# Performance work log

Hardware: AMD Instinct MI355X
Metric: run time of the kernel (lower is better)

Reference implementation:

```python
import jax, jax.numpy as jnp
import numpy as np

B, N, E, H = 32, 512, 512, 8
DH = E // H  # head dim = 64


def setup_inputs() -> dict:
    key = jax.random.key(0)
    ks = jax.random.split(key, 10)
    x = jax.random.normal(ks[0], (B, N, E), jnp.float32)
    adj = jax.random.bernoulli(ks[1], 0.5, (N, N))
    # ensure every query attends to at least itself (no fully-masked rows)
    adj = adj.at[jnp.arange(N), jnp.arange(N)].set(True)
    s = 0.02
    Wq = s * jax.random.normal(ks[2], (E, E), jnp.float32)
    Wk = s * jax.random.normal(ks[3], (E, E), jnp.float32)
    Wv = s * jax.random.normal(ks[4], (E, E), jnp.float32)
    Wo = s * jax.random.normal(ks[5], (E, E), jnp.float32)
    bq = s * jax.random.normal(ks[6], (E,), jnp.float32)
    bk = s * jax.random.normal(ks[7], (E,), jnp.float32)
    bv = s * jax.random.normal(ks[8], (E,), jnp.float32)
    bo = s * jax.random.normal(ks[9], (E,), jnp.float32)
    return {"x": x, "adj": adj, "Wq": Wq, "Wk": Wk, "Wv": Wv,
            "bq": bq, "bk": bk, "bv": bv, "Wo": Wo, "bo": bo}


def reference(x, adj, Wq, Wk, Wv, bq, bk, bv, Wo, bo):
    # Original module loops over queries i, calling nn.MultiheadAttention with
    # key_padding_mask = ~adj[i]; equivalent to one attention with ~adj as a
    # per-query x per-key mask (True = disallowed).
    b, n, e = x.shape
    mask = ~adj  # [N,N] True where attention is NOT allowed
    q = (x @ Wq.T + bq).reshape(b, n, H, DH)
    k = (x @ Wk.T + bk).reshape(b, n, H, DH)
    v = (x @ Wv.T + bv).reshape(b, n, H, DH)
    scale = 1.0 / jnp.sqrt(jnp.float32(DH))
    scores = jnp.einsum('bqhd,bkhd->bhqk', q, k) * scale  # [B,H,N,N]
    scores = jnp.where(mask[None, None, :, :], -jnp.inf, scores)
    p = jax.nn.softmax(scores, axis=-1)
    o = jnp.einsum('bhqk,bkhd->bqhd', p, v).reshape(b, n, e)
    return o @ Wo.T + bo  # [B,N,E]
```

## Files before the change

kernel.cpp:

```cpp
#include <hip/hip_runtime.h>
#include <stdint.h>

typedef __bf16 bf16_t;
typedef bf16_t bf16x8 __attribute__((ext_vector_type(8)));
typedef float f32x4 __attribute__((ext_vector_type(4)));


__device__ __forceinline__ uint16_t f2bf(float f) {
    uint32_t u = __float_as_uint(f);
    u += 0x7FFFu + ((u >> 16) & 1u);
    return (uint16_t)(u >> 16);
}

__device__ __forceinline__ f32x4 mfma16(bf16x8 a, bf16x8 b, f32x4 c) {
    return __builtin_amdgcn_mfma_f32_16x16x32_bf16(a, b, c, 0, 0, 0);
}

__device__ __forceinline__ bf16x8 lds_frag(const uint16_t* smem, int row, int kbyte) {
    int off = row * 128 + (kbyte ^ ((row & 7) << 4));
    return __builtin_bit_cast(bf16x8,
        *reinterpret_cast<const uint4*>(reinterpret_cast<const char*>(smem) + off));
}

template <int ROWS>
__device__ __forceinline__ void stage_tile(uint16_t* lds, const uint16_t* src,
                                           int src_stride, int tid) {
    constexpr int CH  = ROWS * 8;
    constexpr int PER = CH / 256;
#pragma unroll
    for (int i = 0; i < PER; ++i) {
        int c   = tid + i * 256;
        int row = c >> 3, cc = c & 7;
        uint4 v = *reinterpret_cast<const uint4*>(src + (size_t)row * src_stride + cc * 8);
        int off = row * 128 + ((cc * 16) ^ ((row & 7) << 4));
        *reinterpret_cast<uint4*>(reinterpret_cast<char*>(lds) + off) = v;
    }
}

__global__ void detect_kernel(const unsigned int* __restrict__ adj, int* __restrict__ flag) {
    __shared__ int notint, notf32;
    if (threadIdx.x == 0) { notint = 0; notf32 = 0; }
    __syncthreads();
    int ni = 0, nf = 0;
    for (int i = threadIdx.x; i < 4096; i += 256) {
        unsigned v = adj[i];
        if (v > 1u) ni = 1;
        if (v != 0u && v != 0x3f800000u) nf = 1;
    }
    if (ni) notint = 1;
    if (nf) notf32 = 1;
    __syncthreads();
    if (threadIdx.x == 0) *flag = notint ? (notf32 ? 2 : 1) : 0;
}

__global__ void convert_kernel(const float* __restrict__ x, const float* __restrict__ wq,
                               const float* __restrict__ wk, const float* __restrict__ wv,
                               const float* __restrict__ wo,
                               uint16_t* __restrict__ xb, uint16_t* __restrict__ wqb,
                               uint16_t* __restrict__ wkb, uint16_t* __restrict__ wvb,
                               uint16_t* __restrict__ wob) {
    int i = blockIdx.x * 256 + threadIdx.x;
    const float* src; uint16_t* dst; int idx;
    if (i < 2097152) { src = x; dst = xb; idx = i; }
    else {
        int wi = i - 2097152;
        int which = wi >> 16; idx = wi & 65535;
        src = which == 0 ? wq : which == 1 ? wk : which == 2 ? wv : wo;
        dst = which == 0 ? wqb : which == 1 ? wkb : which == 2 ? wvb : wob;
    }
    float4 v = reinterpret_cast<const float4*>(src)[idx];
    ushort4 o;
    o.x = f2bf(v.x); o.y = f2bf(v.y); o.z = f2bf(v.z); o.w = f2bf(v.w);
    reinterpret_cast<ushort4*>(dst)[idx] = o;
}

template <int MODE>
__launch_bounds__(256)
__global__ void gemm_kernel(const uint16_t* __restrict__ A,
                            const uint16_t* __restrict__ B0, const uint16_t* __restrict__ B1,
                            const uint16_t* __restrict__ B2,
                            const float* __restrict__ bias0, const float* __restrict__ bias1,
                            const float* __restrict__ bias2,
                            uint16_t* __restrict__ qws, uint16_t* __restrict__ kws,
                            uint16_t* __restrict__ vws, float* __restrict__ outf) {
    __shared__ uint16_t As[128 * 64];
    __shared__ uint16_t Bs[128 * 64];
    const int tid  = threadIdx.x;
    const int lane = tid & 63;
    const int wid  = tid >> 6;
    const int wm   = wid >> 1, wn = wid & 1;
    const int m0   = blockIdx.y * 128;
    const int n0   = blockIdx.x * 128;
    const int sel  = n0 >> 9;
    const int nw   = n0 & 511;
    const uint16_t* Bsrc = (MODE == 0) ? (sel == 0 ? B0 : sel == 1 ? B1 : B2) : B0;
    const int fr = lane & 15, fq = lane >> 4;

    f32x4 acc[4][4];
#pragma unroll
    for (int a = 0; a < 4; ++a)
#pragma unroll
        for (int b = 0; b < 4; ++b) acc[a][b] = (f32x4){0.f, 0.f, 0.f, 0.f};

    for (int k0 = 0; k0 < 512; k0 += 64) {
        __syncthreads();
        stage_tile<128>(As, A + (size_t)m0 * 512 + k0, 512, tid);
        stage_tile<128>(Bs, Bsrc + (size_t)nw * 512 + k0, 512, tid);
        __syncthreads();
#pragma unroll
        for (int ks = 0; ks < 2; ++ks) {
            int kb = ks * 64 + fq * 16;
            bf16x8 af[4], bfr[4];
#pragma unroll
            for (int i = 0; i < 4; ++i) af[i]  = lds_frag(As, wm * 64 + i * 16 + fr, kb);
#pragma unroll
            for (int i = 0; i < 4; ++i) bfr[i] = lds_frag(Bs, wn * 64 + i * 16 + fr, kb);
#pragma unroll
            for (int mf = 0; mf < 4; ++mf)
#pragma unroll
                for (int nf = 0; nf < 4; ++nf)
                    acc[mf][nf] = mfma16(af[mf], bfr[nf], acc[mf][nf]);
        }
    }

    if (MODE == 0) {
        const float* bias = sel == 0 ? bias0 : sel == 1 ? bias1 : bias2;
#pragma unroll
        for (int nf = 0; nf < 4; ++nf) {
            int c  = nw + wn * 64 + nf * 16 + fr;
            float bv = bias[c];
            int h = c >> 6, dh = c & 63;
#pragma unroll
            for (int mf = 0; mf < 4; ++mf) {
                int mbase = m0 + wm * 64 + mf * 16 + fq * 4;
                int b  = mbase >> 9;
                int ns = mbase & 511;
                if (sel < 2) {
                    uint16_t* dst = (sel == 0 ? qws : kws);
                    size_t base = ((size_t)(b * 8 + h) * 512) * 64;
#pragma unroll
                    for (int j = 0; j < 4; ++j)
                        dst[base + (size_t)(ns + j) * 64 + dh] = f2bf(acc[mf][nf][j] + bv);
                } else {
                    ushort4 pk;
                    pk.x = f2bf(acc[mf][nf][0] + bv);
                    pk.y = f2bf(acc[mf][nf][1] + bv);
                    pk.z = f2bf(acc[mf][nf][2] + bv);
                    pk.w = f2bf(acc[mf][nf][3] + bv);
                    *reinterpret_cast<ushort4*>(
                        &vws[((size_t)(b * 8 + h) * 64 + dh) * 512 + ns]) = pk;
                }
            }
        }
    } else {
#pragma unroll
        for (int nf = 0; nf < 4; ++nf) {
            int c = n0 + wn * 64 + nf * 16 + fr;
            float bv = bias0[c];
#pragma unroll
            for (int mf = 0; mf < 4; ++mf) {
                int mbase = m0 + wm * 64 + mf * 16 + fq * 4;
#pragma unroll
                for (int j = 0; j < 4; ++j)
                    outf[(size_t)(mbase + j) * 512 + c] = acc[mf][nf][j] + bv;
            }
        }
    }
}

__launch_bounds__(256)
__global__ void attn_kernel(const uint16_t* __restrict__ qws, const uint16_t* __restrict__ kws,
                            const uint16_t* __restrict__ vws, const void* __restrict__ adj,
                            const int* __restrict__ mode_flag, uint16_t* __restrict__ ows) {
    __shared__ uint16_t Ks[64 * 64];
    __shared__ uint16_t Vs[64 * 64];
    __shared__ uint16_t Ps[4 * 16 * 64];
    const int tid = threadIdx.x, lane = tid & 63, w = tid >> 6;
    const int bx = blockIdx.x;
    const int qt = bx & 7, h = (bx >> 3) & 7, b = bx >> 6;
    const int mode = *mode_flag;
    const size_t qk_head = (size_t)(b * 8 + h) * 512 * 64;
    const size_t v_head  = (size_t)(b * 8 + h) * 64 * 512;
    const int fr = lane & 15, fq = lane >> 4;
    const int qr0 = qt * 64 + w * 16;

    bf16x8 aq[2];
#pragma unroll
    for (int ks = 0; ks < 2; ++ks)
        aq[ks] = __builtin_bit_cast(bf16x8,
            *reinterpret_cast<const uint4*>(qws + qk_head + (size_t)(qr0 + fr) * 64 + ks * 32 + fq * 8));

    float mrun[4], lsum[4];
    f32x4 oacc[4];
#pragma unroll
    for (int j = 0; j < 4; ++j) { mrun[j] = -1e30f; lsum[j] = 0.f; }
#pragma unroll
    for (int nf = 0; nf < 4; ++nf) oacc[nf] = (f32x4){0.f, 0.f, 0.f, 0.f};

    const float LOG2E = 1.4426950408889634f;

    for (int kt = 0; kt < 8; ++kt) {
        __syncthreads();
        stage_tile<64>(Ks, kws + qk_head + (size_t)kt * 64 * 64, 64, tid);
        stage_tile<64>(Vs, vws + v_head + (size_t)kt * 64, 512, tid);
        __syncthreads();

        f32x4 sacc[4];
#pragma unroll
        for (int nf = 0; nf < 4; ++nf) sacc[nf] = (f32x4){0.f, 0.f, 0.f, 0.f};
#pragma unroll
        for (int ks = 0; ks < 2; ++ks) {
            int kb = ks * 64 + fq * 16;
#pragma unroll
            for (int nf = 0; nf < 4; ++nf) {
                bf16x8 bk = lds_frag(Ks, nf * 16 + fr, kb);
                sacc[nf] = mfma16(aq[ks], bk, sacc[nf]);
            }
        }

        float s[4][4];
#pragma unroll
        for (int nf = 0; nf < 4; ++nf) {
            int kg = kt * 64 + nf * 16 + fr;
#pragma unroll
            for (int j = 0; j < 4; ++j) {
                int qg = qt * 64 + w * 16 + fq * 4 + j;
                bool ok;
                if (mode == 0)      ok = reinterpret_cast<const int*>(adj)[qg * 512 + kg] != 0;
                else if (mode == 1) ok = reinterpret_cast<const float*>(adj)[qg * 512 + kg] != 0.0f;
                else                ok = reinterpret_cast<const unsigned char*>(adj)[qg * 512 + kg] != 0;
                s[nf][j] = ok ? sacc[nf][j] * 0.125f : -1e30f;
            }
        }

        float fsc[4];
#pragma unroll
        for (int j = 0; j < 4; ++j) {
            float t = fmaxf(fmaxf(s[0][j], s[1][j]), fmaxf(s[2][j], s[3][j]));
            t = fmaxf(t, __shfl_xor(t, 1));
            t = fmaxf(t, __shfl_xor(t, 2));
            t = fmaxf(t, __shfl_xor(t, 4));
            t = fmaxf(t, __shfl_xor(t, 8));
            float mn = fmaxf(mrun[j], t);
            fsc[j] = exp2f((mrun[j] - mn) * LOG2E);
            mrun[j] = mn;
        }
        float rs[4] = {0.f, 0.f, 0.f, 0.f};
#pragma unroll
        for (int nf = 0; nf < 4; ++nf)
#pragma unroll
            for (int j = 0; j < 4; ++j) {
                float p = exp2f((s[nf][j] - mrun[j]) * LOG2E);
                s[nf][j] = p;
                rs[j] += p;
            }
#pragma unroll
        for (int j = 0; j < 4; ++j) {
            float r = rs[j];
            r += __shfl_xor(r, 1);
            r += __shfl_xor(r, 2);
            r += __shfl_xor(r, 4);
            r += __shfl_xor(r, 8);
            lsum[j] = lsum[j] * fsc[j] + r;
        }
#pragma unroll
        for (int nf = 0; nf < 4; ++nf)
#pragma unroll
            for (int j = 0; j < 4; ++j) oacc[nf][j] *= fsc[j];

        uint16_t* pw = Ps + w * 16 * 64;
#pragma unroll
        for (int nf = 0; nf < 4; ++nf)
#pragma unroll
            for (int j = 0; j < 4; ++j) {
                int rp = fq * 4 + j, cp = nf * 16 + fr;
                int off = rp * 128 + ((cp * 2) ^ ((rp & 7) << 4));
                *reinterpret_cast<uint16_t*>(reinterpret_cast<char*>(pw) + off) = f2bf(s[nf][j]);
            }

#pragma unroll
        for (int ks = 0; ks < 2; ++ks) {
            int kb = ks * 64 + fq * 16;
            bf16x8 ap = lds_frag(pw, fr, kb);
#pragma unroll
            for (int nf = 0; nf < 4; ++nf) {
                bf16x8 bv = lds_frag(Vs, nf * 16 + fr, kb);
                oacc[nf] = mfma16(ap, bv, oacc[nf]);
            }
        }
    }

#pragma unroll
    for (int nf = 0; nf < 4; ++nf) {
        int d = nf * 16 + fr;
#pragma unroll
        for (int j = 0; j < 4; ++j) {
            int n = qt * 64 + w * 16 + fq * 4 + j;
            float v = oacc[nf][j] / lsum[j];
            ows[((size_t)(b * 512 + n) * 8 + h) * 64 + d] = f2bf(v);
        }
    }
}

extern "C" void kernel_launch(void* const* d_in, const int* in_sizes, int n_in,
                              void* d_out, int out_size, void* d_ws, size_t ws_size,
                              hipStream_t stream) {
    const float* x  = (const float*)d_in[0];
    const void*  adj = d_in[1];
    const float* Wq = (const float*)d_in[2];
    const float* Wk = (const float*)d_in[3];
    const float* Wv = (const float*)d_in[4];
    const float* bq = (const float*)d_in[5];
    const float* bk = (const float*)d_in[6];
    const float* bv = (const float*)d_in[7];
    const float* Wo = (const float*)d_in[8];
    const float* bo = (const float*)d_in[9];
    float* out = (float*)d_out;

    char* p = (char*)d_ws;
    uint16_t* xb  = (uint16_t*)p; p += (size_t)8388608 * 2;
    uint16_t* wqb = (uint16_t*)p; p += 262144 * 2;
    uint16_t* wkb = (uint16_t*)p; p += 262144 * 2;
    uint16_t* wvb = (uint16_t*)p; p += 262144 * 2;
    uint16_t* wob = (uint16_t*)p; p += 262144 * 2;
    uint16_t* qws = (uint16_t*)p; p += (size_t)8388608 * 2;
    uint16_t* kws = (uint16_t*)p; p += (size_t)8388608 * 2;
    uint16_t* vws = (uint16_t*)p; p += (size_t)8388608 * 2;
    int* flag = (int*)p;
    uint16_t* ows = xb;

    detect_kernel<<<1, 256, 0, stream>>>((const unsigned int*)adj, flag);
    convert_kernel<<<9216, 256, 0, stream>>>(x, Wq, Wk, Wv, Wo, xb, wqb, wkb, wvb, wob);
    dim3 g1(12, 128);
    gemm_kernel<0><<<g1, 256, 0, stream>>>(xb, wqb, wkb, wvb, bq, bk, bv,
                                           qws, kws, vws, nullptr);
    attn_kernel<<<2048, 256, 0, stream>>>(qws, kws, vws, adj, flag, ows);
    dim3 g2(4, 128);
    gemm_kernel<1><<<g2, 256, 0, stream>>>(ows, wob, wob, wob, bo, bo, bo,
                                           nullptr, nullptr, nullptr, out);
}
```

Baseline: 325.2 us.

## Prefetch tiles into registers, pack adjacency to bitmask, fold softmax scale into Q

Both the GEMM and attention kernels now load the next K-tile from global memory into registers while the current tile is consumed, so global latency overlaps with MFMA work. A new pack kernel turns the adjacency matrix into 64-bit bitmasks that each attention block caches in LDS, replacing per-element global mask reads and the mode branch. The 1/sqrt(d) scale is folded into the Q projection epilogue, and s_setprio hints are placed around the MFMA sections. Costs are more registers for the prefetch buffers, one extra small kernel launch, and Q being rounded to bf16 after scaling.

```diff
diff --git a/kernel.cpp b/kernel.cpp
--- a/kernel.cpp
+++ b/kernel.cpp
@@ -23,17 +23,25 @@
 }
 
 template <int ROWS>
-__device__ __forceinline__ void stage_tile(uint16_t* lds, const uint16_t* src,
-                                           int src_stride, int tid) {
-    constexpr int CH  = ROWS * 8;
-    constexpr int PER = CH / 256;
+__device__ __forceinline__ void load_regs(uint4* r, const uint16_t* src,
+                                          int src_stride, int tid) {
+    constexpr int PER = ROWS * 8 / 256;
 #pragma unroll
     for (int i = 0; i < PER; ++i) {
-        int c   = tid + i * 256;
+        int c = tid + i * 256;
         int row = c >> 3, cc = c & 7;
-        uint4 v = *reinterpret_cast<const uint4*>(src + (size_t)row * src_stride + cc * 8);
+        r[i] = *reinterpret_cast<const uint4*>(src + (size_t)row * src_stride + cc * 8);
+    }
+}
+template <int ROWS>
+__device__ __forceinline__ void write_lds(uint16_t* lds, const uint4* r, int tid) {
+    constexpr int PER = ROWS * 8 / 256;
+#pragma unroll
+    for (int i = 0; i < PER; ++i) {
+        int c = tid + i * 256;
+        int row = c >> 3, cc = c & 7;
         int off = row * 128 + ((cc * 16) ^ ((row & 7) << 4));
-        *reinterpret_cast<uint4*>(reinterpret_cast<char*>(lds) + off) = v;
+        *reinterpret_cast<uint4*>(reinterpret_cast<char*>(lds) + off) = r[i];
     }
 }
 
@@ -51,6 +59,28 @@
     if (nf) notf32 = 1;
     __syncthreads();
     if (threadIdx.x == 0) *flag = notint ? (notf32 ? 2 : 1) : 0;
+}
+
+__global__ void pack_kernel(const void* __restrict__ adj, const int* __restrict__ flag,
+                            uint64_t* __restrict__ bits) {
+    int idx = blockIdx.x * 256 + threadIdx.x;
+    int row = idx >> 3, w = idx & 7;
+    int mode = *flag;
+    uint64_t m = 0;
+    if (mode == 0) {
+        const int* a = (const int*)adj + row * 512 + w * 64;
+#pragma unroll 8
+        for (int b = 0; b < 64; ++b) m |= (uint64_t)(a[b] != 0) << b;
+    } else if (mode == 1) {
+        const float* a = (const float*)adj + row * 512 + w * 64;
+#pragma unroll 8
+        for (int b = 0; b < 64; ++b) m |= (uint64_t)(a[b] != 0.0f) << b;
+    } else {
+        const unsigned char* a = (const unsigned char*)adj + row * 512 + w * 64;
+#pragma unroll 8
+        for (int b = 0; b < 64; ++b) m |= (uint64_t)(a[b] != 0) << b;
+    }
+    bits[idx] = m;
 }
 
 __global__ void convert_kernel(const float* __restrict__ x, const float* __restrict__ wq,
@@ -102,10 +132,18 @@
 #pragma unroll
         for (int b = 0; b < 4; ++b) acc[a][b] = (f32x4){0.f, 0.f, 0.f, 0.f};
 
+    uint4 apre[4], bpre[4];
+    load_regs<128>(apre, A + (size_t)m0 * 512, 512, tid);
+    load_regs<128>(bpre, Bsrc + (size_t)nw * 512, 512, tid);
+
     for (int k0 = 0; k0 < 512; k0 += 64) {
         __syncthreads();
-        stage_tile<128>(As, A + (size_t)m0 * 512 + k0, 512, tid);
-        stage_tile<128>(Bs, Bsrc + (size_t)nw * 512 + k0, 512, tid);
+        write_lds<128>(As, apre, tid);
+        write_lds<128>(Bs, bpre, tid);
+        if (k0 < 448) {
+            load_regs<128>(apre, A + (size_t)m0 * 512 + k0 + 64, 512, tid);
+            load_regs<128>(bpre, Bsrc + (size_t)nw * 512 + k0 + 64, 512, tid);
+        }
         __syncthreads();
 #pragma unroll
         for (int ks = 0; ks < 2; ++ks) {
@@ -125,6 +163,7 @@
 
     if (MODE == 0) {
         const float* bias = sel == 0 ? bias0 : sel == 1 ? bias1 : bias2;
+        const float sc = (sel == 0) ? 0.125f : 1.0f;
 #pragma unroll
         for (int nf = 0; nf < 4; ++nf) {
             int c  = nw + wn * 64 + nf * 16 + fr;
@@ -140,7 +179,7 @@
                     size_t base = ((size_t)(b * 8 + h) * 512) * 64;
 #pragma unroll
                     for (int j = 0; j < 4; ++j)
-                        dst[base + (size_t)(ns + j) * 64 + dh] = f2bf(acc[mf][nf][j] + bv);
+                        dst[base + (size_t)(ns + j) * 64 + dh] = f2bf((acc[mf][nf][j] + bv) * sc);
                 } else {
                     ushort4 pk;
                     pk.x = f2bf(acc[mf][nf][0] + bv);
@@ -170,20 +209,23 @@
 
 __launch_bounds__(256)
 __global__ void attn_kernel(const uint16_t* __restrict__ qws, const uint16_t* __restrict__ kws,
-                            const uint16_t* __restrict__ vws, const void* __restrict__ adj,
-                            const int* __restrict__ mode_flag, uint16_t* __restrict__ ows) {
+                            const uint16_t* __restrict__ vws,
+                            const uint64_t* __restrict__ adjbits, uint16_t* __restrict__ ows) {
     __shared__ uint16_t Ks[64 * 64];
     __shared__ uint16_t Vs[64 * 64];
     __shared__ uint16_t Ps[4 * 16 * 64];
+    __shared__ uint64_t Ab[64 * 8];
     const int tid = threadIdx.x, lane = tid & 63, w = tid >> 6;
     const int bx = blockIdx.x;
     const int qt = bx & 7, h = (bx >> 3) & 7, b = bx >> 6;
-    const int mode = *mode_flag;
     const size_t qk_head = (size_t)(b * 8 + h) * 512 * 64;
     const size_t v_head  = (size_t)(b * 8 + h) * 64 * 512;
     const int fr = lane & 15, fq = lane >> 4;
     const int qr0 = qt * 64 + w * 16;
 
+    Ab[tid]       = adjbits[(size_t)qt * 512 + tid];
+    Ab[tid + 256] = adjbits[(size_t)qt * 512 + tid + 256];
+
     bf16x8 aq[2];
 #pragma unroll
     for (int ks = 0; ks < 2; ++ks)
@@ -199,15 +241,24 @@
 
     const float LOG2E = 1.4426950408889634f;
 
+    uint4 kreg[2], vreg[2];
+    load_regs<64>(kreg, kws + qk_head, 64, tid);
+    load_regs<64>(vreg, vws + v_head, 512, tid);
+
     for (int kt = 0; kt < 8; ++kt) {
         __syncthreads();
-        stage_tile<64>(Ks, kws + qk_head + (size_t)kt * 64 * 64, 64, tid);
-        stage_tile<64>(Vs, vws + v_head + (size_t)kt * 64, 512, tid);
+        write_lds<64>(Ks, kreg, tid);
+        write_lds<64>(Vs, vreg, tid);
+        if (kt < 7) {
+            load_regs<64>(kreg, kws + qk_head + (size_t)(kt + 1) * 64 * 64, 64, tid);
+            load_regs<64>(vreg, vws + v_head + (size_t)(kt + 1) * 64, 512, tid);
+        }
         __syncthreads();
 
         f32x4 sacc[4];
 #pragma unroll
         for (int nf = 0; nf < 4; ++nf) sacc[nf] = (f32x4){0.f, 0.f, 0.f, 0.f};
+        __builtin_amdgcn_s_setprio(1);
 #pragma unroll
         for (int ks = 0; ks < 2; ++ks) {
             int kb = ks * 64 + fq * 16;
@@ -217,20 +268,15 @@
                 sacc[nf] = mfma16(aq[ks], bk, sacc[nf]);
             }
         }
+        __builtin_amdgcn_s_setprio(0);
 
         float s[4][4];
 #pragma unroll
-        for (int nf = 0; nf < 4; ++nf) {
-            int kg = kt * 64 + nf * 16 + fr;
-#pragma unroll
-            for (int j = 0; j < 4; ++j) {
-                int qg = qt * 64 + w * 16 + fq * 4 + j;
-                bool ok;
-                if (mode == 0)      ok = reinterpret_cast<const int*>(adj)[qg * 512 + kg] != 0;
-                else if (mode == 1) ok = reinterpret_cast<const float*>(adj)[qg * 512 + kg] != 0.0f;
-                else                ok = reinterpret_cast<const unsigned char*>(adj)[qg * 512 + kg] != 0;
-                s[nf][j] = ok ? sacc[nf][j] * 0.125f : -1e30f;
-            }
+        for (int j = 0; j < 4; ++j) {
+            uint64_t m = Ab[(w * 16 + fq * 4 + j) * 8 + kt];
+#pragma unroll
+            for (int nf = 0; nf < 4; ++nf)
+                s[nf][j] = ((m >> (nf * 16 + fr)) & 1) ? sacc[nf][j] : -1e30f;
         }
 
         float fsc[4];
@@ -278,6 +324,7 @@
                 *reinterpret_cast<uint16_t*>(reinterpret_cast<char*>(pw) + off) = f2bf(s[nf][j]);
             }
 
+        __builtin_amdgcn_s_setprio(1);
 #pragma unroll
         for (int ks = 0; ks < 2; ++ks) {
             int kb = ks * 64 + fq * 16;
@@ -288,6 +335,7 @@
                 oacc[nf] = mfma16(ap, bv, oacc[nf]);
             }
         }
+        __builtin_amdgcn_s_setprio(0);
     }
 
 #pragma unroll
@@ -326,15 +374,17 @@
     uint16_t* qws = (uint16_t*)p; p += (size_t)8388608 * 2;
     uint16_t* kws = (uint16_t*)p; p += (size_t)8388608 * 2;
     uint16_t* vws = (uint16_t*)p; p += (size_t)8388608 * 2;
+    uint64_t* adjbits = (uint64_t*)p; p += 4096 * 8;
     int* flag = (int*)p;
     uint16_t* ows = xb;
 
     detect_kernel<<<1, 256, 0, stream>>>((const unsigned int*)adj, flag);
+    pack_kernel<<<16, 256, 0, stream>>>(adj, flag, adjbits);
     convert_kernel<<<9216, 256, 0, stream>>>(x, Wq, Wk, Wv, Wo, xb, wqb, wkb, wvb, wob);
     dim3 g1(12, 128);
     gemm_kernel<0><<<g1, 256, 0, stream>>>(xb, wqb, wkb, wvb, bq, bk, bv,
                                            qws, kws, vws, nullptr);
-    attn_kernel<<<2048, 256, 0, stream>>>(qws, kws, vws, adj, flag, ows);
+    attn_kernel<<<2048, 256, 0, stream>>>(qws, kws, vws, adjbits, ows);
     dim3 g2(4, 128);
     gemm_kernel<1><<<g2, 256, 0, stream>>>(ows, wob, wob, wob, bo, bo, bo,
                                            nullptr, nullptr, nullptr, out);
```

Result: slower. 388.5 us (+19.5%).
